# Performance work log

Hardware: AMD Instinct MI355X
Metric: run time of the kernel (lower is better)

The kernel has to match this reference:

```python
import jax, jax.numpy as jnp
import numpy as np

AC_KERNEL = 5


def deconv(x, w, stride):
    """torch ConvTranspose2d(k=3, p=1, bias=False), stride 1 or 2 (output_padding=1).
    w has torch layout [Cin, Cout, kH, kW]."""
    wk = jnp.transpose(w, (1, 0, 2, 3))[:, :, ::-1, ::-1]  # OIHW, spatially flipped
    dn = ('NCHW', 'OIHW', 'NCHW')
    if stride == 1:
        return jax.lax.conv_general_dilated(x, wk, (1, 1), ((1, 1), (1, 1)), dimension_numbers=dn)
    # stride 2: dilate input, pad (k-1-p, k-1-p+op) = (1, 2) -> doubles H, W
    return jax.lax.conv_general_dilated(x, wk, (1, 1), ((1, 2), (1, 2)),
                                        lhs_dilation=(2, 2), dimension_numbers=dn)


def sepconv(feat, kv, kh, K):
    """Per-pixel adaptive separable convolution (Niklaus SepConv).
    feat: [B,C,H,W]; kv, kh: [B,K,H,W]. Replication-pad by K//2, then
    out[b,c,y,x] = sum_{i,j} pad[b,c,y+i,x+j] * kv[b,i,y,x] * kh[b,j,y,x]."""
    pad = K // 2
    B, C, H, W = feat.shape
    p = jnp.pad(feat, ((0, 0), (0, 0), (pad, pad), (pad, pad)), mode='edge')
    out = jnp.zeros_like(feat)
    for i in range(K):  # small fixed loop over kernel taps
        row = p[:, :, i:i + H, :]  # [B,C,H,W+2*pad]
        horiz = row[:, :, :, 0:W] * kh[:, 0:1]
        for j in range(1, K):
            horiz = horiz + row[:, :, :, j:j + W] * kh[:, j:j + 1]
        out = out + kv[:, i:i + 1] * horiz
    return out


def fusion(feat, kv, kh, mask):
    tmp = sepconv(feat, kv, kh, AC_KERNEL)
    return mask * tmp + (1.0 - mask) * feat


def setup_inputs() -> dict:
    key = jax.random.key(0)
    ks = jax.random.split(key, 20)
    B, G = 128, 64
    d = {'cont_feat': jax.random.normal(ks[0], (B, G, 8, 8), jnp.float32)}
    sizes = [8, 16, 32, 64]
    for li, s in enumerate(sizes):
        d[f'kv{li}'] = jax.random.uniform(ks[1 + 3 * li], (B, AC_KERNEL, s, s), jnp.float32)
        d[f'kh{li}'] = jax.random.uniform(ks[2 + 3 * li], (B, AC_KERNEL, s, s), jnp.float32)
        d[f'm{li}'] = jax.random.uniform(ks[3 + 3 * li], (B, 1, s, s), jnp.float32)
    wshapes = [(G, G * 8, 3, 3), (G * 8, G * 4, 3, 3), (G * 4, G * 2, 3, 3),
               (G * 2, G * 2, 3, 3), (G * 2, G, 3, 3), (G, 3, 3, 3)]
    for wi, ws in enumerate(wshapes):
        d[f'w{wi + 1}'] = jax.random.normal(ks[13 + wi], ws, jnp.float32) * 0.05
    return d


def reference(cont_feat, kv0, kh0, m0, kv1, kh1, m1, kv2, kh2, m2, kv3, kh3, m3,
              w1, w2, w3, w4, w5, w6):
    # kernel_layer = 4, no_mask = False, use_bn = False
    feat_8 = fusion(cont_feat, kv0, kh0, m0)                      # [B,G,8,8]
    feat_16 = jax.nn.relu(deconv(feat_8, w1, 2))                  # [B,8G,16,16]
    feat_16 = fusion(feat_16, kv1, kh1, m1)
    h = jax.nn.relu(deconv(feat_16, w2, 1))                       # [B,4G,16,16]
    feat_32 = jax.nn.relu(deconv(h, w3, 2))                       # [B,2G,32,32]
    feat_32 = fusion(feat_32, kv2, kh2, m2)
    h = jax.nn.relu(deconv(feat_32, w4, 1))                       # [B,2G,32,32]
    h = jax.nn.relu(deconv(h, w5, 2))                             # [B,G,64,64]
    out = jnp.tanh(deconv(h, w6, 1))                              # [B,3,64,64]
    out = fusion(out, kv3, kh3, m3)
    return (out, feat_8, feat_16, feat_32)
```

## Files before the change

kernel.cpp:

```cpp
#include <hip/hip_runtime.h>
#include <math.h>

typedef short v8s __attribute__((ext_vector_type(8)));
typedef float v16f __attribute__((ext_vector_type(16)));

__device__ inline unsigned short f2bf(float f) {
    union { float f; unsigned u; } c; c.f = f;
    unsigned r = (c.u + 0x7fffu + ((c.u >> 16) & 1u)) >> 16;
    return (unsigned short)r;
}

template<int LW, int CH>
__global__ __launch_bounds__(256) void fusion2_kernel(
        const float* __restrict__ feat, const float* __restrict__ kv,
        const float* __restrict__ kh, const float* __restrict__ m,
        float* __restrict__ out, unsigned short* __restrict__ xout,
        int C, int H, int lhw) {
    constexpr int W = 1 << LW;
    const int t = blockIdx.x * 256 + threadIdx.x;
    const int hw = H << LW;
    const int b = t >> lhw;
    const int pix = t & (hw - 1);
    const int x = pix & (W - 1);
    const int y = pix >> LW;
    const int lane = threadIdx.x & 63;
    const int rowbase = (lane & ~(W - 1)) << 2;

    const int c0 = blockIdx.y * CH;

    const float mv = m[(size_t)b * hw + pix];
    float kvv[5], khv[5];
#pragma unroll
    for (int i = 0; i < 5; i++) {
        kvv[i] = kv[((size_t)b * 5 + i) * hw + pix];
        khv[i] = kh[((size_t)b * 5 + i) * hw + pix];
    }
    int idx[5];
#pragma unroll
    for (int j = 0; j < 5; j++) {
        int xx = x + j - 2; xx = xx < 0 ? 0 : (xx >= W ? W - 1 : xx);
        idx[j] = rowbase + (xx << 2);
    }
    int roff[5];
#pragma unroll
    for (int i = 0; i < 5; i++) {
        int yy = y + i - 2; yy = yy < 0 ? 0 : (yy >= H ? H - 1 : yy);
        roff[i] = (yy << LW) + x;
    }

    const float* fbase = feat + ((size_t)b * C + c0) * hw;
    float* obase = out + ((size_t)b * C + c0) * hw + pix;
    const float om = 1.f - mv;

    unsigned pk[(CH + 1) / 2];
#pragma unroll
    for (int i = 0; i < (CH + 1) / 2; i++) pk[i] = 0u;

#pragma unroll
    for (int cc = 0; cc < CH; cc++) {
        const float* q = fbase + (size_t)cc * hw;
        float s = 0.f;
        float fv = 0.f;
#pragma unroll
        for (int i = 0; i < 5; i++) {
            float v = q[roff[i]];
            if (i == 2) fv = v;
            int vb = __float_as_int(v);
            float h = 0.f;
#pragma unroll
            for (int j = 0; j < 5; j++) {
                float nv = __int_as_float(
                    __builtin_amdgcn_ds_bpermute(idx[j], vb));
                h += nv * khv[j];
            }
            s += kvv[i] * h;
        }
        float r = mv * s + om * fv;
        obase[(size_t)cc * hw] = r;
        if constexpr (CH == 16)
            pk[cc >> 1] |= (unsigned)f2bf(r) << ((cc & 1) * 16);
    }
    if constexpr (CH == 16) {
        if (xout) {
            unsigned short* xp = xout + ((size_t)b * hw + pix) * C + c0;
            *(uint4*)(xp)     = make_uint4(pk[0], pk[1], pk[2], pk[3]);
            *(uint4*)(xp + 8) = make_uint4(pk[4], pk[5], pk[6], pk[7]);
        }
    }
}

__global__ __launch_bounds__(256) void nchw_to_nhwc_bf16(
        const float* __restrict__ in, unsigned short* __restrict__ out,
        int C, int H, int W, int lw, int lc2) {
    extern __shared__ unsigned short sm_t[];
    const int y = blockIdx.x, b = blockIdx.y;
    const int Cp = C + 8;
    const int tid = threadIdx.x;
    for (int i = tid; i < C * W; i += 256) {
        int x = i & (W - 1), c = i >> lw;
        float v = in[(((size_t)b * C + c) * H + y) * W + x];
        sm_t[x * Cp + c] = f2bf(v);
    }
    __syncthreads();
    const unsigned* s32 = (const unsigned*)sm_t;
    unsigned* o32 = (unsigned*)(out + (((size_t)b * H + y) * W) * C);
    const int n32 = (W * C) >> 1;
    for (int i = tid; i < n32; i += 256) {
        int x = i >> lc2;
        int c2 = i - (x << lc2);
        o32[i] = s32[x * (Cp >> 1) + c2];
    }
}

__global__ __launch_bounds__(256) void repack_w_frag(
        const float* __restrict__ w, unsigned short* __restrict__ wk,
        int Cin, int Cout, int flip) {
    int idx = blockIdx.x * 256 + threadIdx.x;
    if (idx >= Cin * Cout) return;
    int ci = idx / Cout, co = idx - ci * Cout;
    const float* src = w + (size_t)idx * 9;
    const int nCb = Cout >> 5, nH = Cin >> 4;
    const size_t inner = (size_t)((((ci >> 3) & 1) * 32 + (co & 31)) * 8 + (ci & 7));
#pragma unroll
    for (int k = 0; k < 9; k++) {
        int t = flip ? (8 - k) : k;
        size_t blk = ((size_t)t * nCb + (co >> 5)) * nH + (ci >> 4);
        wk[(blk << 9) + inner] = f2bf(src[k]);
    }
}

template<int W, int TH, int LW>
__global__ __launch_bounds__(256) void conv3x3_mfma(
        const unsigned short* __restrict__ X,
        const unsigned short* __restrict__ Wk,
        unsigned short* __restrict__ out, int Cin, int Cout, int H) {
    constexpr int TP = (TH + 2) * (W + 2);
    constexpr int NIT = TP * 4;
    constexpr int NLD = (NIT + 255) / 256;
    __shared__ unsigned short sB[2][TP * 40];
    const int tid = threadIdx.x;
    const int lane = tid & 63, wv = tid >> 6;
    const int wm = wv >> 1, wn = wv & 1;
    const int y0 = blockIdx.x * TH;
    const int coB = blockIdx.y * 128 + wm * 64;
    const int b = blockIdx.z;
    const int n = lane & 31, kg = lane >> 5;
    const int p0 = wn * 64 + n, p1 = p0 + 32;
    const int r0 = p0 >> LW, c0 = p0 & (W - 1);
    const int r1 = p1 >> LW, c1 = p1 & (W - 1);
    const int bo0 = (r0 * (W + 2) + c0) * 40 + kg * 8;
    const int bo1 = (r1 * (W + 2) + c1) * 40 + kg * 8;
    v16f acc00 = {}, acc01 = {}, acc10 = {}, acc11 = {};
    const size_t cbStride = (size_t)(Cin >> 4) << 9;
    const size_t tStride  = (size_t)(Cout >> 5) * cbStride;
    const unsigned short* Af = Wk + (size_t)(coB >> 5) * cbStride + (lane << 3);
    const unsigned short* Xb = X + (size_t)b * H * W * Cin;

    const unsigned short* ldp[NLD];
    int sto[NLD];
#pragma unroll
    for (int s = 0; s < NLD; s++) {
        int i = tid + s * 256;
        bool slot = (i < NIT);
        int pix = i >> 2, part = i & 3;
        int py = pix / (W + 2), px = pix - py * (W + 2);
        int gy = y0 + py - 1, gx = px - 1;
        bool ok = slot && gy >= 0 && gy < H && (unsigned)gx < (unsigned)W;
        ldp[s] = ok ? Xb + ((size_t)(gy * W + gx)) * Cin + part * 8 : nullptr;
        sto[s] = slot ? pix * 40 + part * 8 : -1;
    }

    uint4 pre[NLD];
#pragma unroll
    for (int s = 0; s < NLD; s++)
        pre[s] = ldp[s] ? *(const uint4*)(ldp[s]) : make_uint4(0u, 0u, 0u, 0u);
#pragma unroll
    for (int s = 0; s < NLD; s++)
        if (sto[s] >= 0) *(uint4*)(sB[0] + sto[s]) = pre[s];
    __syncthreads();

    const int NK = Cin >> 5;
    for (int kk = 0; kk < NK; kk++) {
        const int cur = kk & 1;
        const int ci0 = kk << 5;
        const bool more = (kk + 1 < NK);
        if (more) {
#pragma unroll
            for (int s = 0; s < NLD; s++)
                pre[s] = ldp[s] ? *(const uint4*)(ldp[s] + ci0 + 32)
                                : make_uint4(0u, 0u, 0u, 0u);
        }
        const unsigned short* sC = sB[cur];
#pragma unroll
        for (int t = 0; t < 9; t++) {
            const int ky = t / 3, kx = t - ky * 3;
            const int toff = (ky * (W + 2) + kx) * 40;
#pragma unroll
            for (int kh = 0; kh < 2; kh++) {
                const unsigned short* ap =
                    Af + (size_t)t * tStride + (size_t)(((ci0 >> 4) + kh) << 9);
                v8s A0 = *(const v8s*)(ap);
                v8s A1 = *(const v8s*)(ap + cbStride);
                v8s B0 = *(const v8s*)(sC + bo0 + toff + kh * 16);
                v8s B1 = *(const v8s*)(sC + bo1 + toff + kh * 16);
                acc00 = __builtin_amdgcn_mfma_f32_32x32x16_bf16(A0, B0, acc00, 0, 0, 0);
                acc01 = __builtin_amdgcn_mfma_f32_32x32x16_bf16(A0, B1, acc01, 0, 0, 0);
                acc10 = __builtin_amdgcn_mfma_f32_32x32x16_bf16(A1, B0, acc10, 0, 0, 0);
                acc11 = __builtin_amdgcn_mfma_f32_32x32x16_bf16(A1, B1, acc11, 0, 0, 0);
            }
        }
        if (more) {
            unsigned short* sN = sB[cur ^ 1];
#pragma unroll
            for (int s = 0; s < NLD; s++)
                if (sto[s] >= 0) *(uint4*)(sN + sto[s]) = pre[s];
            __syncthreads();
        }
    }
    unsigned short* ob = out + (size_t)b * H * W * Cout;
#pragma unroll
    for (int sm = 0; sm < 2; sm++) {
        v16f a0 = sm ? acc10 : acc00;
        v16f a1 = sm ? acc11 : acc01;
        const int cobase = coB + sm * 32 + 4 * kg;
        unsigned short* q0p = ob + ((size_t)((y0 + r0) * W + c0)) * Cout + cobase;
        unsigned short* q1p = ob + ((size_t)((y0 + r1) * W + c1)) * Cout + cobase;
#pragma unroll
        for (int r2 = 0; r2 < 4; r2++) {
            ushort4 q0, q1; float v;
            v = a0[4 * r2 + 0]; v = v > 0.f ? v : 0.f; q0.x = f2bf(v);
            v = a0[4 * r2 + 1]; v = v > 0.f ? v : 0.f; q0.y = f2bf(v);
            v = a0[4 * r2 + 2]; v = v > 0.f ? v : 0.f; q0.z = f2bf(v);
            v = a0[4 * r2 + 3]; v = v > 0.f ? v : 0.f; q0.w = f2bf(v);
            *(ushort4*)(q0p + 8 * r2) = q0;
            v = a1[4 * r2 + 0]; v = v > 0.f ? v : 0.f; q1.x = f2bf(v);
            v = a1[4 * r2 + 1]; v = v > 0.f ? v : 0.f; q1.y = f2bf(v);
            v = a1[4 * r2 + 2]; v = v > 0.f ? v : 0.f; q1.z = f2bf(v);
            v = a1[4 * r2 + 3]; v = v > 0.f ? v : 0.f; q1.w = f2bf(v);
            *(ushort4*)(q1p + 8 * r2) = q1;
        }
    }
}

template<int W, int TH, int NWN, int NWM, int LW>
__global__ __launch_bounds__(256) void deconv2_mfma(
        const unsigned short* __restrict__ X,
        const unsigned short* __restrict__ Wk,
        float* __restrict__ out, int Cin, int Cout, int Hin) {
    constexpr int ROWS = NWN * TH + 1;
    constexpr int NPIX = ROWS * (W + 1);
    constexpr int NIT = NPIX * 4;
    constexpr int NLD = (NIT + 255) / 256;
    __shared__ unsigned short sB[2][NPIX * 40];
    const int tid = threadIdx.x;
    const int lane = tid & 63, wv = tid >> 6;
    const int wm = wv / NWN, wn = wv % NWN;
    const int n = lane & 31, kg = lane >> 5;
    const int y0 = blockIdx.x * (NWN * TH);
    const int coB = (blockIdx.y * NWM + wm) * 64;
    const int b = blockIdx.z;
    const int Yl = wn * TH + (n >> LW);
    const int Xl = n & (W - 1);
    v16f zero = {};
    v16f acc[2][2][2];
#pragma unroll
    for (int i = 0; i < 2; i++)
#pragma unroll
        for (int j = 0; j < 2; j++)
#pragma unroll
            for (int s = 0; s < 2; s++) acc[i][j][s] = zero;
    const unsigned short* Xb = X + (size_t)b * Hin * W * Cin;
    const size_t cbStride = (size_t)(Cin >> 4) << 9;
    const size_t tStride  = (size_t)(Cout >> 5) * cbStride;
    const unsigned short* Af = Wk + (size_t)(coB >> 5) * cbStride + (lane << 3);
    const int PY[3] = {1, 0, 1}, DY[3] = {1, 0, 0};

    const unsigned short* ldp[NLD];
    int sto[NLD];
#pragma unroll
    for (int s = 0; s < NLD; s++) {
        int i = tid + s * 256;
        bool slot = (i < NIT);
        int pix = i >> 2, part = i & 3;
        int py_ = pix / (W + 1), px_ = pix - py_ * (W + 1);
        int gy = y0 + py_, gx = px_;
        bool ok = slot && gy < Hin && gx < W;
        ldp[s] = ok ? Xb + ((size_t)(gy * W + gx)) * Cin + part * 8 : nullptr;
        sto[s] = slot ? pix * 40 + part * 8 : -1;
    }

    uint4 pre[NLD];
#pragma unroll
    for (int s = 0; s < NLD; s++)
        pre[s] = ldp[s] ? *(const uint4*)(ldp[s]) : make_uint4(0u, 0u, 0u, 0u);
#pragma unroll
    for (int s = 0; s < NLD; s++)
        if (sto[s] >= 0) *(uint4*)(sB[0] + sto[s]) = pre[s];
    __syncthreads();

    const int NK = Cin >> 5;
    for (int kk = 0; kk < NK; kk++) {
        const int cur = kk & 1;
        const int ci0 = kk << 5;
        const bool more = (kk + 1 < NK);
        if (more) {
#pragma unroll
            for (int s = 0; s < NLD; s++)
                pre[s] = ldp[s] ? *(const uint4*)(ldp[s] + ci0 + 32)
                                : make_uint4(0u, 0u, 0u, 0u);
        }
        const unsigned short* sC = sB[cur];
#pragma unroll
        for (int ky = 0; ky < 3; ky++) {
#pragma unroll
            for (int kx = 0; kx < 3; kx++) {
                const int py = PY[ky], dy = DY[ky];
                const int px = PY[kx], dx = DY[kx];
                const int t = ky * 3 + kx;
                const int boff = ((Yl + dy) * (W + 1) + (Xl + dx)) * 40 + kg * 8;
#pragma unroll
                for (int kh = 0; kh < 2; kh++) {
                    const unsigned short* ap =
                        Af + (size_t)t * tStride + (size_t)(((ci0 >> 4) + kh) << 9);
                    v8s B  = *(const v8s*)(sC + boff + kh * 16);
                    v8s A0 = *(const v8s*)(ap);
                    v8s A1 = *(const v8s*)(ap + cbStride);
                    acc[py][px][0] = __builtin_amdgcn_mfma_f32_32x32x16_bf16(A0, B, acc[py][px][0], 0, 0, 0);
                    acc[py][px][1] = __builtin_amdgcn_mfma_f32_32x32x16_bf16(A1, B, acc[py][px][1], 0, 0, 0);
                }
            }
        }
        if (more) {
            unsigned short* sN = sB[cur ^ 1];
#pragma unroll
            for (int s = 0; s < NLD; s++)
                if (sto[s] >= 0) *(uint4*)(sN + sto[s]) = pre[s];
            __syncthreads();
        }
    }
    const int Wo = 2 * W, Ho = 2 * Hin;
    const int yin = y0 + Yl;
#pragma unroll
    for (int py = 0; py < 2; py++) {
        const int oy = 2 * yin + py;
#pragma unroll
        for (int sm = 0; sm < 2; sm++) {
            const int cobase = coB + sm * 32 + 4 * kg;
#pragma unroll
            for (int r = 0; r < 16; r++) {
                int co = cobase + (r & 3) + 8 * (r >> 2);
                float v0 = acc[py][0][sm][r]; v0 = v0 > 0.f ? v0 : 0.f;
                float v1 = acc[py][1][sm][r]; v1 = v1 > 0.f ? v1 : 0.f;
                *(float2*)(out + (((size_t)(b * Cout + co) * Ho + oy) * Wo + 2 * Xl)) =
                    make_float2(v0, v1);
            }
        }
    }
}

__global__ __launch_bounds__(256) void conv_s1_c3_tanh_kernel(
        const float* __restrict__ in, const float* __restrict__ w,
        float* __restrict__ out, int Cin, int H, int W) {
    __shared__ float sIn[8][18][19];
    __shared__ float sW[8][3][9];
    const int tid = threadIdx.x;
    const int r = tid >> 4, c = tid & 15;
    const int ntx = W >> 4;
    const int tx0 = (blockIdx.x % ntx) << 4, ty0 = (blockIdx.x / ntx) << 4;
    const int b = blockIdx.z;
    const int hw = H * W;
    float acc[3] = {0.f, 0.f, 0.f};
    for (int ci0 = 0; ci0 < Cin; ci0 += 8) {
        for (int i = tid; i < 8 * 18 * 18; i += 256) {
            int ci = i / 324, rr = i % 324, ly = rr / 18, lx = rr % 18;
            int gy = ty0 + ly - 1, gx = tx0 + lx - 1;
            float v = 0.f;
            if (gy >= 0 && gy < H && gx >= 0 && gx < W)
                v = in[(size_t)(b * Cin + ci0 + ci) * hw + gy * W + gx];
            sIn[ci][ly][lx] = v;
        }
        for (int i = tid; i < 8 * 3 * 9; i += 256) {
            int ci = i / 27, rr = i % 27, co = rr / 9, k = rr % 9;
            sW[ci][co][k] = w[(size_t)((ci0 + ci) * 3 + co) * 9 + (8 - k)];
        }
        __syncthreads();
#pragma unroll
        for (int ci = 0; ci < 8; ci++) {
            float v00 = sIn[ci][r][c],     v01 = sIn[ci][r][c + 1],     v02 = sIn[ci][r][c + 2];
            float v10 = sIn[ci][r + 1][c], v11 = sIn[ci][r + 1][c + 1], v12 = sIn[ci][r + 1][c + 2];
            float v20 = sIn[ci][r + 2][c], v21 = sIn[ci][r + 2][c + 1], v22 = sIn[ci][r + 2][c + 2];
#pragma unroll
            for (int co = 0; co < 3; co++) {
                const float* wp = &sW[ci][co][0];
                acc[co] += v00 * wp[0] + v01 * wp[1] + v02 * wp[2]
                         + v10 * wp[3] + v11 * wp[4] + v12 * wp[5]
                         + v20 * wp[6] + v21 * wp[7] + v22 * wp[8];
            }
        }
        __syncthreads();
    }
#pragma unroll
    for (int co = 0; co < 3; co++)
        out[(size_t)(b * 3 + co) * hw + (ty0 + r) * W + tx0 + c] = tanhf(acc[co]);
}

extern "C" void kernel_launch(void* const* d_in, const int* in_sizes, int n_in,
                              void* d_out, int out_size, void* d_ws, size_t ws_size,
                              hipStream_t stream) {
    const float* cont = (const float*)d_in[0];
    const float* kv0 = (const float*)d_in[1];
    const float* kh0 = (const float*)d_in[2];
    const float* m0  = (const float*)d_in[3];
    const float* kv1 = (const float*)d_in[4];
    const float* kh1 = (const float*)d_in[5];
    const float* m1  = (const float*)d_in[6];
    const float* kv2 = (const float*)d_in[7];
    const float* kh2 = (const float*)d_in[8];
    const float* m2  = (const float*)d_in[9];
    const float* kv3 = (const float*)d_in[10];
    const float* kh3 = (const float*)d_in[11];
    const float* m3  = (const float*)d_in[12];
    const float* w1  = (const float*)d_in[13];
    const float* w2  = (const float*)d_in[14];
    const float* w3  = (const float*)d_in[15];
    const float* w4  = (const float*)d_in[16];
    const float* w5  = (const float*)d_in[17];
    const float* w6  = (const float*)d_in[18];

    float* out = (float*)d_out;
    float* f8  = out + 1572864;
    float* f16 = out + 2097152;
    float* f32 = out + 18874368;

    char* ws = (char*)d_ws;

    if (ws_size >= (size_t)102760448) {
        float* A0 = (float*)ws;
        unsigned short* X8  = (unsigned short*)(ws + 67108864);
        unsigned short* Wk1 = (unsigned short*)(ws + 68157440);
        unsigned short* X16 = (unsigned short*)(ws + 69206016);

        fusion2_kernel<3, 16><<<dim3(32, 4), 256, 0, stream>>>(
            cont, kv0, kh0, m0, f8, X8, 64, 8, 6);
        repack_w_frag<<<128, 256, 0, stream>>>(w1, Wk1, 64, 512, 0);
        deconv2_mfma<8, 4, 2, 2, 3><<<dim3(1, 4, 128), 256, 0, stream>>>(
            X8, Wk1, A0, 64, 512, 8);
        fusion2_kernel<4, 16><<<dim3(128, 32), 256, 0, stream>>>(
            A0, kv1, kh1, m1, f16, X16, 512, 16, 8);

        unsigned short* h1b = (unsigned short*)ws;
        unsigned short* Wk2 = (unsigned short*)(ws + 16777216);
        unsigned short* Wk3 = (unsigned short*)(ws + 19136512);
        float* t32 = (float*)(ws + 35651584);
        repack_w_frag<<<512, 256, 0, stream>>>(w2, Wk2, 512, 256, 1);
        conv3x3_mfma<16, 8, 4><<<dim3(2, 2, 128), 256, 0, stream>>>(
            X16, Wk2, h1b, 512, 256, 16);
        repack_w_frag<<<128, 256, 0, stream>>>(w3, Wk3, 256, 128, 0);
        deconv2_mfma<16, 2, 2, 2, 4><<<dim3(4, 1, 128), 256, 0, stream>>>(
            h1b, Wk3, t32, 256, 128, 16);

        unsigned short* Wk4 = (unsigned short*)ws;
        unsigned short* Wk5 = (unsigned short*)(ws + 294912);
        unsigned short* X32 = (unsigned short*)(ws + 524288);
        unsigned short* h2b = (unsigned short*)(ws + 35651584);
        float* h3q = (float*)(ws + 69206016);
        float* tq  = (float*)(ws + 524288);
        repack_w_frag<<<64, 256, 0, stream>>>(w4, Wk4, 128, 128, 1);
        repack_w_frag<<<32, 256, 0, stream>>>(w5, Wk5, 128, 64, 0);
        fusion2_kernel<5, 16><<<dim3(512, 8), 256, 0, stream>>>(
            t32, kv2, kh2, m2, f32, X32, 128, 32, 10);
        conv3x3_mfma<32, 4, 5><<<dim3(8, 1, 128), 256, 0, stream>>>(
            X32, Wk4, h2b, 128, 128, 32);
        for (int q = 0; q < 4; q++) {
            size_t bo = (size_t)q * 32;
            deconv2_mfma<32, 1, 4, 1, 5><<<dim3(8, 1, 32), 256, 0, stream>>>(
                h2b + bo * 131072, Wk5, h3q, 128, 64, 32);
            conv_s1_c3_tanh_kernel<<<dim3(16, 1, 32), 256, 0, stream>>>(h3q, w6, tq, 64, 64, 64);
            fusion2_kernel<6, 3><<<dim3(512, 1), 256, 0, stream>>>(
                tq, kv3 + bo * 5 * 4096, kh3 + bo * 5 * 4096, m3 + bo * 4096,
                out + bo * 3 * 4096, nullptr, 3, 64, 12);
        }
    } else {
        float* A0 = (float*)ws;
        unsigned short* X8  = (unsigned short*)(ws + 67108864);
        unsigned short* Wk1 = (unsigned short*)(ws + 68157440);

        fusion2_kernel<3, 16><<<dim3(32, 4), 256, 0, stream>>>(
            cont, kv0, kh0, m0, f8, nullptr, 64, 8, 6);
        nchw_to_nhwc_bf16<<<dim3(8, 128), 256, 8 * 72 * 2, stream>>>(f8, X8, 64, 8, 8, 3, 5);
        repack_w_frag<<<128, 256, 0, stream>>>(w1, Wk1, 64, 512, 0);
        deconv2_mfma<8, 4, 2, 2, 3><<<dim3(1, 4, 128), 256, 0, stream>>>(
            X8, Wk1, A0, 64, 512, 8);
        fusion2_kernel<4, 16><<<dim3(128, 32), 256, 0, stream>>>(
            A0, kv1, kh1, m1, f16, nullptr, 512, 16, 8);

        unsigned short* X16 = (unsigned short*)ws;
        unsigned short* h1b = (unsigned short*)(ws + 67108864);
        unsigned short* Wk3 = (unsigned short*)(ws + 83886080);
        unsigned short* Wk2 = (unsigned short*)(ws + 84475904);
        nchw_to_nhwc_bf16<<<dim3(16, 128), 256, 16 * 520 * 2, stream>>>(
            f16, X16, 512, 16, 16, 4, 8);
        repack_w_frag<<<512, 256, 0, stream>>>(w2, Wk2, 512, 256, 1);
        conv3x3_mfma<16, 8, 4><<<dim3(2, 2, 128), 256, 0, stream>>>(
            X16, Wk2, h1b, 512, 256, 16);
        repack_w_frag<<<128, 256, 0, stream>>>(w3, Wk3, 256, 128, 0);
        float* t32 = (float*)ws;
        deconv2_mfma<16, 2, 2, 2, 4><<<dim3(4, 1, 128), 256, 0, stream>>>(
            h1b, Wk3, t32, 256, 128, 16);
        fusion2_kernel<5, 16><<<dim3(512, 8), 256, 0, stream>>>(
            t32, kv2, kh2, m2, f32, nullptr, 128, 32, 10);

        unsigned short* Wk4  = (unsigned short*)ws;
        unsigned short* Wk5  = (unsigned short*)(ws + 294912);
        unsigned short* X32q = (unsigned short*)(ws + 524288);
        unsigned short* h2b  = (unsigned short*)(ws + 8912896);
        float* h3q = (float*)(ws + 17301504);
        float* tq  = (float*)(ws + 50855936);
        repack_w_frag<<<64, 256, 0, stream>>>(w4, Wk4, 128, 128, 1);
        repack_w_frag<<<32, 256, 0, stream>>>(w5, Wk5, 128, 64, 0);
        for (int q = 0; q < 4; q++) {
            size_t bo = (size_t)q * 32;
            const float* f32q = f32 + bo * 128 * 1024;
            nchw_to_nhwc_bf16<<<dim3(32, 32), 256, 32 * 136 * 2, stream>>>(
                f32q, X32q, 128, 32, 32, 5, 6);
            conv3x3_mfma<32, 4, 5><<<dim3(8, 1, 32), 256, 0, stream>>>(
                X32q, Wk4, h2b, 128, 128, 32);
            deconv2_mfma<32, 1, 4, 1, 5><<<dim3(8, 1, 32), 256, 0, stream>>>(
                h2b, Wk5, h3q, 128, 64, 32);
            conv_s1_c3_tanh_kernel<<<dim3(16, 1, 32), 256, 0, stream>>>(h3q, w6, tq, 64, 64, 64);
            fusion2_kernel<6, 3><<<dim3(512, 1), 256, 0, stream>>>(
                tq, kv3 + bo * 5 * 4096, kh3 + bo * 5 * 4096, m3 + bo * 4096,
                out + bo * 3 * 4096, nullptr, 3, 64, 12);
        }
    }
}
```

Measured before the change: 933.8 us.

## Double conv3x3 pixel tile per wave and shrink LDS pixel stride

The stride-1 conv kernel now gives each wave four 32-pixel fragments instead of two, so every A-fragment weight load feeds four MFMAs per output block instead of two. The tile height doubles and the grid halves to match. The LDS per-pixel stride drops from 40 to 36 halfwords in both conv kernels, which shrinks shared memory and changes the bank mapping. Global load pointers become int offsets to cut register use. The eight accumulators raise register pressure and the halved grid lowers parallelism, which may cost occupancy.

Result: slower. 1.028 ms (+10.1%).

```diff
diff --git a/kernel.cpp b/kernel.cpp
--- a/kernel.cpp
+++ b/kernel.cpp
@@ -134,10 +134,11 @@
         const unsigned short* __restrict__ X,
         const unsigned short* __restrict__ Wk,
         unsigned short* __restrict__ out, int Cin, int Cout, int H) {
+    constexpr int PS = 36;
     constexpr int TP = (TH + 2) * (W + 2);
     constexpr int NIT = TP * 4;
     constexpr int NLD = (NIT + 255) / 256;
-    __shared__ unsigned short sB[2][TP * 40];
+    __shared__ unsigned short sB[2][TP * PS];
     const int tid = threadIdx.x;
     const int lane = tid & 63, wv = tid >> 6;
     const int wm = wv >> 1, wn = wv & 1;
@@ -145,19 +146,24 @@
     const int coB = blockIdx.y * 128 + wm * 64;
     const int b = blockIdx.z;
     const int n = lane & 31, kg = lane >> 5;
-    const int p0 = wn * 64 + n, p1 = p0 + 32;
-    const int r0 = p0 >> LW, c0 = p0 & (W - 1);
-    const int r1 = p1 >> LW, c1 = p1 & (W - 1);
-    const int bo0 = (r0 * (W + 2) + c0) * 40 + kg * 8;
-    const int bo1 = (r1 * (W + 2) + c1) * 40 + kg * 8;
-    v16f acc00 = {}, acc01 = {}, acc10 = {}, acc11 = {};
+    int bo[4], pr[4], pc[4];
+#pragma unroll
+    for (int f = 0; f < 4; f++) {
+        int p = wn * 128 + f * 32 + n;
+        pr[f] = p >> LW; pc[f] = p & (W - 1);
+        bo[f] = (pr[f] * (W + 2) + pc[f]) * PS + kg * 8;
+    }
+    v16f acc[2][4];
+#pragma unroll
+    for (int i = 0; i < 2; i++)
+#pragma unroll
+        for (int f = 0; f < 4; f++) acc[i][f] = (v16f){};
     const size_t cbStride = (size_t)(Cin >> 4) << 9;
     const size_t tStride  = (size_t)(Cout >> 5) * cbStride;
     const unsigned short* Af = Wk + (size_t)(coB >> 5) * cbStride + (lane << 3);
     const unsigned short* Xb = X + (size_t)b * H * W * Cin;
 
-    const unsigned short* ldp[NLD];
-    int sto[NLD];
+    int off[NLD], sto[NLD];
 #pragma unroll
     for (int s = 0; s < NLD; s++) {
         int i = tid + s * 256;
@@ -166,14 +172,15 @@
         int py = pix / (W + 2), px = pix - py * (W + 2);
         int gy = y0 + py - 1, gx = px - 1;
         bool ok = slot && gy >= 0 && gy < H && (unsigned)gx < (unsigned)W;
-        ldp[s] = ok ? Xb + ((size_t)(gy * W + gx)) * Cin + part * 8 : nullptr;
-        sto[s] = slot ? pix * 40 + part * 8 : -1;
+        off[s] = ok ? (gy * W + gx) * Cin + part * 8 : -1;
+        sto[s] = slot ? pix * PS + part * 8 : -1;
     }
 
     uint4 pre[NLD];
 #pragma unroll
     for (int s = 0; s < NLD; s++)
-        pre[s] = ldp[s] ? *(const uint4*)(ldp[s]) : make_uint4(0u, 0u, 0u, 0u);
+        pre[s] = (off[s] >= 0) ? *(const uint4*)(Xb + off[s])
+                               : make_uint4(0u, 0u, 0u, 0u);
 #pragma unroll
     for (int s = 0; s < NLD; s++)
         if (sto[s] >= 0) *(uint4*)(sB[0] + sto[s]) = pre[s];
@@ -187,26 +194,26 @@
         if (more) {
 #pragma unroll
             for (int s = 0; s < NLD; s++)
-                pre[s] = ldp[s] ? *(const uint4*)(ldp[s] + ci0 + 32)
-                                : make_uint4(0u, 0u, 0u, 0u);
+                pre[s] = (off[s] >= 0) ? *(const uint4*)(Xb + off[s] + ci0 + 32)
+                                       : make_uint4(0u, 0u, 0u, 0u);
         }
         const unsigned short* sC = sB[cur];
 #pragma unroll
         for (int t = 0; t < 9; t++) {
             const int ky = t / 3, kx = t - ky * 3;
-            const int toff = (ky * (W + 2) + kx) * 40;
+            const int toff = (ky * (W + 2) + kx) * PS;
 #pragma unroll
             for (int kh = 0; kh < 2; kh++) {
                 const unsigned short* ap =
                     Af + (size_t)t * tStride + (size_t)(((ci0 >> 4) + kh) << 9);
                 v8s A0 = *(const v8s*)(ap);
                 v8s A1 = *(const v8s*)(ap + cbStride);
-                v8s B0 = *(const v8s*)(sC + bo0 + toff + kh * 16);
-                v8s B1 = *(const v8s*)(sC + bo1 + toff + kh * 16);
-                acc00 = __builtin_amdgcn_mfma_f32_32x32x16_bf16(A0, B0, acc00, 0, 0, 0);
-                acc01 = __builtin_amdgcn_mfma_f32_32x32x16_bf16(A0, B1, acc01, 0, 0, 0);
-                acc10 = __builtin_amdgcn_mfma_f32_32x32x16_bf16(A1, B0, acc10, 0, 0, 0);
-                acc11 = __builtin_amdgcn_mfma_f32_32x32x16_bf16(A1, B1, acc11, 0, 0, 0);
+#pragma unroll
+                for (int f = 0; f < 4; f++) {
+                    v8s B = *(const v8s*)(sC + bo[f] + toff + kh * 16);
+                    acc[0][f] = __builtin_amdgcn_mfma_f32_32x32x16_bf16(A0, B, acc[0][f], 0, 0, 0);
+                    acc[1][f] = __builtin_amdgcn_mfma_f32_32x32x16_bf16(A1, B, acc[1][f], 0, 0, 0);
+                }
             }
         }
         if (more) {
@@ -220,24 +227,20 @@
     unsigned short* ob = out + (size_t)b * H * W * Cout;
 #pragma unroll
     for (int sm = 0; sm < 2; sm++) {
-        v16f a0 = sm ? acc10 : acc00;
-        v16f a1 = sm ? acc11 : acc01;
         const int cobase = coB + sm * 32 + 4 * kg;
-        unsigned short* q0p = ob + ((size_t)((y0 + r0) * W + c0)) * Cout + cobase;
-        unsigned short* q1p = ob + ((size_t)((y0 + r1) * W + c1)) * Cout + cobase;
-#pragma unroll
-        for (int r2 = 0; r2 < 4; r2++) {
-            ushort4 q0, q1; float v;
-            v = a0[4 * r2 + 0]; v = v > 0.f ? v : 0.f; q0.x = f2bf(v);
-            v = a0[4 * r2 + 1]; v = v > 0.f ? v : 0.f; q0.y = f2bf(v);
-            v = a0[4 * r2 + 2]; v = v > 0.f ? v : 0.f; q0.z = f2bf(v);
-            v = a0[4 * r2 + 3]; v = v > 0.f ? v : 0.f; q0.w = f2bf(v);
-            *(ushort4*)(q0p + 8 * r2) = q0;
-            v = a1[4 * r2 + 0]; v = v > 0.f ? v : 0.f; q1.x = f2bf(v);
-            v = a1[4 * r2 + 1]; v = v > 0.f ? v : 0.f; q1.y = f2bf(v);
-            v = a1[4 * r2 + 2]; v = v > 0.f ? v : 0.f; q1.z = f2bf(v);
-            v = a1[4 * r2 + 3]; v = v > 0.f ? v : 0.f; q1.w = f2bf(v);
-            *(ushort4*)(q1p + 8 * r2) = q1;
+#pragma unroll
+        for (int f = 0; f < 4; f++) {
+            unsigned short* qp =
+                ob + ((size_t)((y0 + pr[f]) * W + pc[f])) * Cout + cobase;
+#pragma unroll
+            for (int r2 = 0; r2 < 4; r2++) {
+                ushort4 q0; float v;
+                v = acc[sm][f][4 * r2 + 0]; v = v > 0.f ? v : 0.f; q0.x = f2bf(v);
+                v = acc[sm][f][4 * r2 + 1]; v = v > 0.f ? v : 0.f; q0.y = f2bf(v);
+                v = acc[sm][f][4 * r2 + 2]; v = v > 0.f ? v : 0.f; q0.z = f2bf(v);
+                v = acc[sm][f][4 * r2 + 3]; v = v > 0.f ? v : 0.f; q0.w = f2bf(v);
+                *(ushort4*)(qp + 8 * r2) = q0;
+            }
         }
     }
 }
@@ -247,11 +250,12 @@
         const unsigned short* __restrict__ X,
         const unsigned short* __restrict__ Wk,
         float* __restrict__ out, int Cin, int Cout, int Hin) {
+    constexpr int PS = 36;
     constexpr int ROWS = NWN * TH + 1;
     constexpr int NPIX = ROWS * (W + 1);
     constexpr int NIT = NPIX * 4;
     constexpr int NLD = (NIT + 255) / 256;
-    __shared__ unsigned short sB[2][NPIX * 40];
+    __shared__ unsigned short sB[2][NPIX * PS];
     const int tid = threadIdx.x;
     const int lane = tid & 63, wv = tid >> 6;
     const int wm = wv / NWN, wn = wv % NWN;
@@ -275,8 +279,7 @@
     const unsigned short* Af = Wk + (size_t)(coB >> 5) * cbStride + (lane << 3);
     const int PY[3] = {1, 0, 1}, DY[3] = {1, 0, 0};
 
-    const unsigned short* ldp[NLD];
-    int sto[NLD];
+    int off[NLD], sto[NLD];
 #pragma unroll
     for (int s = 0; s < NLD; s++) {
         int i = tid + s * 256;
@@ -285,14 +288,15 @@
         int py_ = pix / (W + 1), px_ = pix - py_ * (W + 1);
         int gy = y0 + py_, gx = px_;
         bool ok = slot && gy < Hin && gx < W;
-        ldp[s] = ok ? Xb + ((size_t)(gy * W + gx)) * Cin + part * 8 : nullptr;
-        sto[s] = slot ? pix * 40 + part * 8 : -1;
+        off[s] = ok ? (gy * W + gx) * Cin + part * 8 : -1;
+        sto[s] = slot ? pix * PS + part * 8 : -1;
     }
 
     uint4 pre[NLD];
 #pragma unroll
     for (int s = 0; s < NLD; s++)
-        pre[s] = ldp[s] ? *(const uint4*)(ldp[s]) : make_uint4(0u, 0u, 0u, 0u);
+        pre[s] = (off[s] >= 0) ? *(const uint4*)(Xb + off[s])
+                               : make_uint4(0u, 0u, 0u, 0u);
 #pragma unroll
     for (int s = 0; s < NLD; s++)
         if (sto[s] >= 0) *(uint4*)(sB[0] + sto[s]) = pre[s];
@@ -306,8 +310,8 @@
         if (more) {
 #pragma unroll
             for (int s = 0; s < NLD; s++)
-                pre[s] = ldp[s] ? *(const uint4*)(ldp[s] + ci0 + 32)
-                                : make_uint4(0u, 0u, 0u, 0u);
+                pre[s] = (off[s] >= 0) ? *(const uint4*)(Xb + off[s] + ci0 + 32)
+                                       : make_uint4(0u, 0u, 0u, 0u);
         }
         const unsigned short* sC = sB[cur];
 #pragma unroll
@@ -317,7 +321,7 @@
                 const int py = PY[ky], dy = DY[ky];
                 const int px = PY[kx], dx = DY[kx];
                 const int t = ky * 3 + kx;
-                const int boff = ((Yl + dy) * (W + 1) + (Xl + dx)) * 40 + kg * 8;
+                const int boff = ((Yl + dy) * (W + 1) + (Xl + dx)) * PS + kg * 8;
 #pragma unroll
                 for (int kh = 0; kh < 2; kh++) {
                     const unsigned short* ap =
@@ -453,7 +457,7 @@
         unsigned short* Wk3 = (unsigned short*)(ws + 19136512);
         float* t32 = (float*)(ws + 35651584);
         repack_w_frag<<<512, 256, 0, stream>>>(w2, Wk2, 512, 256, 1);
-        conv3x3_mfma<16, 8, 4><<<dim3(2, 2, 128), 256, 0, stream>>>(
+        conv3x3_mfma<16, 16, 4><<<dim3(1, 2, 128), 256, 0, stream>>>(
             X16, Wk2, h1b, 512, 256, 16);
         repack_w_frag<<<128, 256, 0, stream>>>(w3, Wk3, 256, 128, 0);
         deconv2_mfma<16, 2, 2, 2, 4><<<dim3(4, 1, 128), 256, 0, stream>>>(
@@ -469,7 +473,7 @@
         repack_w_frag<<<32, 256, 0, stream>>>(w5, Wk5, 128, 64, 0);
         fusion2_kernel<5, 16><<<dim3(512, 8), 256, 0, stream>>>(
             t32, kv2, kh2, m2, f32, X32, 128, 32, 10);
-        conv3x3_mfma<32, 4, 5><<<dim3(8, 1, 128), 256, 0, stream>>>(
+        conv3x3_mfma<32, 8, 5><<<dim3(4, 1, 128), 256, 0, stream>>>(
             X32, Wk4, h2b, 128, 128, 32);
         for (int q = 0; q < 4; q++) {
             size_t bo = (size_t)q * 32;
@@ -501,7 +505,7 @@
         nchw_to_nhwc_bf16<<<dim3(16, 128), 256, 16 * 520 * 2, stream>>>(
             f16, X16, 512, 16, 16, 4, 8);
         repack_w_frag<<<512, 256, 0, stream>>>(w2, Wk2, 512, 256, 1);
-        conv3x3_mfma<16, 8, 4><<<dim3(2, 2, 128), 256, 0, stream>>>(
+        conv3x3_mfma<16, 16, 4><<<dim3(1, 2, 128), 256, 0, stream>>>(
             X16, Wk2, h1b, 512, 256, 16);
         repack_w_frag<<<128, 256, 0, stream>>>(w3, Wk3, 256, 128, 0);
         float* t32 = (float*)ws;
@@ -523,7 +527,7 @@
             const float* f32q = f32 + bo * 128 * 1024;
             nchw_to_nhwc_bf16<<<dim3(32, 32), 256, 32 * 136 * 2, stream>>>(
                 f32q, X32q, 128, 32, 32, 5, 6);
-            conv3x3_mfma<32, 4, 5><<<dim3(8, 1, 32), 256, 0, stream>>>(
+            conv3x3_mfma<32, 8, 5><<<dim3(4, 1, 32), 256, 0, stream>>>(
                 X32q, Wk4, h2b, 128, 128, 32);
             deconv2_mfma<32, 1, 4, 1, 5><<<dim3(8, 1, 32), 256, 0, stream>>>(
                 h2b, Wk5, h3q, 128, 64, 32);
```
